# Kernel tuning notes

Measured on AMD Instinct MI355X. Metric: run time of the kernel, lower is better.

Reference implementation:

```python
import jax, jax.numpy as jnp
import numpy as np

B, N, F_IN, H = 1, 8192, 128, 64
NEG_INF = -1e9


def setup_inputs() -> dict:
    key = jax.random.key(0)
    ks = jax.random.split(key, 6)
    seq = jax.random.normal(ks[0], (B, N, F_IN), dtype=jnp.float32)
    # sparse-ish binary adjacency (~avg degree 64) with self loops
    adj = (jax.random.uniform(ks[1], (B, N, N)) < (64.0 / N)).astype(jnp.float32)
    eye = jnp.eye(N, dtype=jnp.float32)[None]
    adj = jnp.maximum(adj, eye)
    bias_mat = NEG_INF * (1.0 - adj)  # standard GAT bias mask
    W = jax.random.normal(ks[2], (F_IN, H), dtype=jnp.float32) * 0.08
    a1_w = jax.random.normal(ks[3], (H, 1), dtype=jnp.float32) * 0.1
    a2_w = jax.random.normal(ks[4], (H, 1), dtype=jnp.float32) * 0.1
    a1_b = jnp.zeros((1,), dtype=jnp.float32)
    a2_b = jnp.zeros((1,), dtype=jnp.float32)
    bias_zero = jnp.zeros((H,), dtype=jnp.float32)
    return {"seq": seq, "adj": adj, "bias_mat": bias_mat, "W": W,
            "a1_w": a1_w, "a1_b": a1_b, "a2_w": a2_w, "a2_b": a2_b,
            "bias_zero": bias_zero}


def reference(seq, adj, bias_mat, W, a1_w, a1_b, a2_w, a2_b, bias_zero):
    # Conv1D(kernel=1) == per-node linear projection
    seq_fts = jnp.einsum('bnf,fh->bnh', seq, W)          # [B,N,H]
    f1 = jnp.einsum('bnh,ho->bno', seq_fts, a1_w) + a1_b  # [B,N,1]
    f2 = jnp.einsum('bnh,ho->bno', seq_fts, a2_w) + a2_b  # [B,N,1]
    logits = f1 + jnp.swapaxes(f2, 1, 2)                  # [B,N,N] additive GAT logits
    # NOTE: module multiplies leaky_relu(logits) by dense adj, then adds bias_mat
    scores = jax.nn.leaky_relu(logits, 0.2) * adj + bias_mat
    coefs = jax.nn.softmax(scores, axis=-1)               # [B,N,N]
    vals = jnp.einsum('bnm,bmh->bnh', coefs, seq_fts)     # weighted aggregation
    ret = vals + bias_zero
    return jax.nn.elu(ret)
```

## Files before the change

### kernel.cpp

```cpp
#include <hip/hip_runtime.h>
#include <math.h>

#define NN 8192
#define FIN 128
#define HH 64
#define CAP 128
#define PROJ_BLOCKS 512
#define SCAN_BLOCKS 2048

typedef float f32x4 __attribute__((ext_vector_type(4)));
typedef const __attribute__((address_space(1))) unsigned int gu32;
typedef __attribute__((address_space(3))) unsigned int lu32;

__global__ __launch_bounds__(256) void proj_scan_kernel(
    const float* __restrict__ seq, const float* __restrict__ adj,
    const float* __restrict__ W,
    const float* __restrict__ a1_w, const float* __restrict__ a1_b,
    const float* __restrict__ a2_w, const float* __restrict__ a2_b,
    float* __restrict__ seq_fts, float* __restrict__ f1, float* __restrict__ f2,
    int* __restrict__ cnt_g, unsigned short* __restrict__ jb_g)
{
    __shared__ f32x4 stage[4][2][512];

    const int wave = threadIdx.x >> 6;
    const int lane = threadIdx.x & 63;
    const int b    = blockIdx.x;

    if ((b % 5) == 4) {
        const int base = (b / 5) * 16 + wave * 4;
        const float* __restrict__ s0 = seq + (size_t)(base + 0) * FIN;
        const float* __restrict__ s1 = seq + (size_t)(base + 1) * FIN;
        const float* __restrict__ s2 = seq + (size_t)(base + 2) * FIN;
        const float* __restrict__ s3 = seq + (size_t)(base + 3) * FIN;

        float a0 = 0.f, a1 = 0.f, a2 = 0.f, a3 = 0.f;
        #pragma unroll
        for (int f = 0; f < FIN; ++f) {
            const float wf = W[f * HH + lane];
            a0 = fmaf(s0[f], wf, a0);
            a1 = fmaf(s1[f], wf, a1);
            a2 = fmaf(s2[f], wf, a2);
            a3 = fmaf(s3[f], wf, a3);
        }
        seq_fts[(size_t)(base + 0) * HH + lane] = a0;
        seq_fts[(size_t)(base + 1) * HH + lane] = a1;
        seq_fts[(size_t)(base + 2) * HH + lane] = a2;
        seq_fts[(size_t)(base + 3) * HH + lane] = a3;

        const float w1 = a1_w[lane], w2 = a2_w[lane];
        float p10 = a0 * w1, p11 = a1 * w1, p12 = a2 * w1, p13 = a3 * w1;
        float p20 = a0 * w2, p21 = a1 * w2, p22 = a2 * w2, p23 = a3 * w2;
        #pragma unroll
        for (int off = 32; off >= 1; off >>= 1) {
            p10 += __shfl_xor(p10, off, 64);  p11 += __shfl_xor(p11, off, 64);
            p12 += __shfl_xor(p12, off, 64);  p13 += __shfl_xor(p13, off, 64);
            p20 += __shfl_xor(p20, off, 64);  p21 += __shfl_xor(p21, off, 64);
            p22 += __shfl_xor(p22, off, 64);  p23 += __shfl_xor(p23, off, 64);
        }
        if (lane == 0) {
            const float b1 = a1_b[0], b2 = a2_b[0];
            f1[base + 0] = p10 + b1;  f1[base + 1] = p11 + b1;
            f1[base + 2] = p12 + b1;  f1[base + 3] = p13 + b1;
            f2[base + 0] = p20 + b2;  f2[base + 1] = p21 + b2;
            f2[base + 2] = p22 + b2;  f2[base + 3] = p23 + b2;
        }
        return;
    }

    const int row = (b - b / 5) * 4 + wave;
    const char* __restrict__ g = (const char*)(adj + (size_t)row * NN);

    #define ISSUE(C_) do {                                                       \
        const char* src_ = g + (C_) * 8192 + lane * 16;                          \
        f32x4* dst_ = &stage[wave][(C_) & 1][0];                                 \
        _Pragma("unroll")                                                        \
        for (int i_ = 0; i_ < 8; ++i_) {                                         \
            __builtin_amdgcn_global_load_lds((gu32*)(src_ + i_ * 1024),          \
                                             (lu32*)((char*)dst_ + i_ * 1024),   \
                                             16, 0, 0);                          \
        }                                                                        \
    } while (0)

    #define PROCESS(C_, MW_) do {                                                \
        unsigned mw_ = 0;                                                        \
        _Pragma("unroll")                                                        \
        for (int i_ = 0; i_ < 8; ++i_) {                                         \
            const f32x4 a_ = stage[wave][(C_) & 1][i_ * 64 + lane];              \
            const unsigned bits_ = (unsigned)a_.x | ((unsigned)a_.y << 1)        \
                                 | ((unsigned)a_.z << 2) | ((unsigned)a_.w << 3);\
            mw_ |= bits_ << (i_ * 4);                                            \
        }                                                                        \
        (MW_) = mw_;                                                             \
    } while (0)

    #define WAITV(N_) do {                                                       \
        asm volatile("s_waitcnt vmcnt(" #N_ ")" ::: "memory");                   \
        __builtin_amdgcn_sched_barrier(0);                                       \
    } while (0)

    unsigned mask0, mask1, mask2, mask3;
    ISSUE(0); ISSUE(1);
    WAITV(8);
    PROCESS(0, mask0);
    __builtin_amdgcn_sched_barrier(0);
    ISSUE(2);
    WAITV(8);
    PROCESS(1, mask1);
    __builtin_amdgcn_sched_barrier(0);
    ISSUE(3);
    WAITV(8);
    PROCESS(2, mask2);
    WAITV(0);
    PROCESS(3, mask3);

    const int cnt = __popc(mask0) + __popc(mask1) + __popc(mask2) + __popc(mask3);
    int incl = cnt;
    #pragma unroll
    for (int off = 1; off < 64; off <<= 1) {
        const int u = __shfl_up(incl, off, 64);
        if (lane >= off) incl += u;
    }
    if (lane == 63) cnt_g[row] = incl;
    int p = incl - cnt;

    unsigned short* __restrict__ jrow = jb_g + (size_t)row * CAP;
    #define DECODE(MW, W_) do {                                              \
        unsigned m_ = (MW);                                                  \
        while (m_) {                                                         \
            const int b_ = __builtin_ctz(m_);  m_ &= m_ - 1;                 \
            const int j_ = ((((W_) * 8 + (b_ >> 2)) * 64 + lane) << 2) + (b_ & 3); \
            if (p < CAP) jrow[p] = (unsigned short)j_;                       \
            ++p;                                                             \
        }                                                                    \
    } while (0)
    DECODE(mask0, 0); DECODE(mask1, 1); DECODE(mask2, 2); DECODE(mask3, 3);
    #undef DECODE
    #undef ISSUE
    #undef PROCESS
    #undef WAITV
}

__global__ __launch_bounds__(256, 6) void gather_kernel(
    const float* __restrict__ seq_fts, const float* __restrict__ f1,
    const float* __restrict__ f2, const int* __restrict__ cnt_g,
    const unsigned short* __restrict__ jb_g,
    const float* __restrict__ bias_zero, float* __restrict__ out)
{
    const int wave = threadIdx.x >> 6;
    const int lane = threadIdx.x & 63;
    const int row  = blockIdx.x * 4 + wave;

    __shared__ int   jbuf[4][CAP];
    __shared__ float sbuf[4][CAP];

    const int n = min(cnt_g[row], CAP);
    const float f1i = f1[row];
    const unsigned short* __restrict__ jrow = jb_g + (size_t)row * CAP;

    float m = -1e30f;
    for (int q = lane; q < n; q += 64) {
        const int j = jrow[q];
        jbuf[wave][q] = j;
        const float x = f1i + f2[j];
        const float s = (x >= 0.f) ? x : 0.2f * x;
        sbuf[wave][q] = s;
        m = fmaxf(m, s);
    }
    #pragma unroll
    for (int off = 32; off >= 1; off >>= 1) m = fmaxf(m, __shfl_xor(m, off, 64));

    float d = 0.f;
    for (int q = lane; q < n; q += 64) {
        const float e = __expf(sbuf[wave][q] - m);
        sbuf[wave][q] = e;
        d += e;
    }
    #pragma unroll
    for (int off = 32; off >= 1; off >>= 1) d += __shfl_xor(d, off, 64);

    float acc0 = 0.f, acc1 = 0.f, acc2 = 0.f, acc3 = 0.f;
    float acc4 = 0.f, acc5 = 0.f, acc6 = 0.f, acc7 = 0.f;
    int q = 0;
    for (; q + 7 < n; q += 8) {
        acc0 = fmaf(sbuf[wave][q+0], seq_fts[(size_t)jbuf[wave][q+0] * HH + lane], acc0);
        acc1 = fmaf(sbuf[wave][q+1], seq_fts[(size_t)jbuf[wave][q+1] * HH + lane], acc1);
        acc2 = fmaf(sbuf[wave][q+2], seq_fts[(size_t)jbuf[wave][q+2] * HH + lane], acc2);
        acc3 = fmaf(sbuf[wave][q+3], seq_fts[(size_t)jbuf[wave][q+3] * HH + lane], acc3);
        acc4 = fmaf(sbuf[wave][q+4], seq_fts[(size_t)jbuf[wave][q+4] * HH + lane], acc4);
        acc5 = fmaf(sbuf[wave][q+5], seq_fts[(size_t)jbuf[wave][q+5] * HH + lane], acc5);
        acc6 = fmaf(sbuf[wave][q+6], seq_fts[(size_t)jbuf[wave][q+6] * HH + lane], acc6);
        acc7 = fmaf(sbuf[wave][q+7], seq_fts[(size_t)jbuf[wave][q+7] * HH + lane], acc7);
    }
    for (; q < n; ++q)
        acc0 = fmaf(sbuf[wave][q], seq_fts[(size_t)jbuf[wave][q] * HH + lane], acc0);

    const float v = (((acc0 + acc1) + (acc2 + acc3)) + ((acc4 + acc5) + (acc6 + acc7))) / d
                    + bias_zero[lane];
    out[(size_t)row * HH + lane] = (v > 0.f) ? v : expm1f(v);
}

extern "C" void kernel_launch(void* const* d_in, const int* in_sizes, int n_in,
                              void* d_out, int out_size, void* d_ws, size_t ws_size,
                              hipStream_t stream) {
    const float* seq       = (const float*)d_in[0];
    const float* adj       = (const float*)d_in[1];
    const float* W         = (const float*)d_in[3];
    const float* a1_w      = (const float*)d_in[4];
    const float* a1_b      = (const float*)d_in[5];
    const float* a2_w      = (const float*)d_in[6];
    const float* a2_b      = (const float*)d_in[7];
    const float* bias_zero = (const float*)d_in[8];
    float* out = (float*)d_out;

    char* ws = (char*)d_ws;
    float* seq_fts        = (float*)ws;
    float* f1             = (float*)(ws + 2097152);
    float* f2             = (float*)(ws + 2097152 + 32768);
    int*   cnt_g          = (int*)  (ws + 2097152 + 65536);
    unsigned short* jb_g  = (unsigned short*)(ws + 2097152 + 98304);

    proj_scan_kernel<<<PROJ_BLOCKS + SCAN_BLOCKS, 256, 0, stream>>>(
        seq, adj, W, a1_w, a1_b, a2_w, a2_b, seq_fts, f1, f2, cnt_g, jb_g);
    gather_kernel<<<NN / 4, 256, 0, stream>>>(
        seq_fts, f1, f2, cnt_g, jb_g, bias_zero, out);
}
```

Before: 61.44 us.

## Halve adjacency scan chunk size and deepen pipeline to eight stages

The adjacency row scan now stages 4 KB chunks per wave instead of 8 KB, halving the LDS footprint. It runs an eight-stage double-buffered pipeline and sets a nontemporal cache-policy bit on the global-to-LDS loads. Launch bounds now request 4 blocks per CU, aiming at higher occupancy and more loads in flight across waves for this bandwidth-bound scan. In exchange each wave has less per-wave load depth and more wait/process steps, and the bitmask decode index formula is rewritten to match the new chunk layout.

Result: slower. 69.89 us (+13.8%).

```diff
diff --git a/kernel.cpp b/kernel.cpp
--- a/kernel.cpp
+++ b/kernel.cpp
@@ -12,7 +12,7 @@
 typedef const __attribute__((address_space(1))) unsigned int gu32;
 typedef __attribute__((address_space(3))) unsigned int lu32;
 
-__global__ __launch_bounds__(256) void proj_scan_kernel(
+__global__ __launch_bounds__(256, 4) void proj_scan_kernel(
     const float* __restrict__ seq, const float* __restrict__ adj,
     const float* __restrict__ W,
     const float* __restrict__ a1_w, const float* __restrict__ a1_b,
@@ -20,7 +20,7 @@
     float* __restrict__ seq_fts, float* __restrict__ f1, float* __restrict__ f2,
     int* __restrict__ cnt_g, unsigned short* __restrict__ jb_g)
 {
-    __shared__ f32x4 stage[4][2][512];
+    __shared__ f32x4 stage[4][2][256];
 
     const int wave = threadIdx.x >> 6;
     const int lane = threadIdx.x & 63;
@@ -71,47 +71,49 @@
     const char* __restrict__ g = (const char*)(adj + (size_t)row * NN);
 
     #define ISSUE(C_) do {                                                       \
-        const char* src_ = g + (C_) * 8192 + lane * 16;                          \
-        f32x4* dst_ = &stage[wave][(C_) & 1][0];                                 \
+        const char* src_ = g + (C_) * 4096 + lane * 16;                          \
+        char* dst_ = (char*)&stage[wave][(C_) & 1][0];                           \
         _Pragma("unroll")                                                        \
-        for (int i_ = 0; i_ < 8; ++i_) {                                         \
+        for (int i_ = 0; i_ < 4; ++i_) {                                         \
             __builtin_amdgcn_global_load_lds((gu32*)(src_ + i_ * 1024),          \
-                                             (lu32*)((char*)dst_ + i_ * 1024),   \
-                                             16, 0, 0);                          \
+                                             (lu32*)(dst_ + i_ * 1024),          \
+                                             16, 0, 2 );                   \
         }                                                                        \
     } while (0)
 
-    #define PROCESS(C_, MW_) do {                                                \
-        unsigned mw_ = 0;                                                        \
+    #define PROCESS(C_, HW_) do {                                                \
+        unsigned hw_ = 0;                                                        \
         _Pragma("unroll")                                                        \
-        for (int i_ = 0; i_ < 8; ++i_) {                                         \
+        for (int i_ = 0; i_ < 4; ++i_) {                                         \
             const f32x4 a_ = stage[wave][(C_) & 1][i_ * 64 + lane];              \
             const unsigned bits_ = (unsigned)a_.x | ((unsigned)a_.y << 1)        \
                                  | ((unsigned)a_.z << 2) | ((unsigned)a_.w << 3);\
-            mw_ |= bits_ << (i_ * 4);                                            \
+            hw_ |= bits_ << (i_ * 4);                                            \
         }                                                                        \
-        (MW_) = mw_;                                                             \
+        (HW_) = hw_;                                                             \
     } while (0)
 
     #define WAITV(N_) do {                                                       \
         asm volatile("s_waitcnt vmcnt(" #N_ ")" ::: "memory");                   \
         __builtin_amdgcn_sched_barrier(0);                                       \
     } while (0)
-
-    unsigned mask0, mask1, mask2, mask3;
+    #define SB __builtin_amdgcn_sched_barrier(0)
+
+    unsigned h0, h1, h2, h3, h4, h5, h6, h7;
     ISSUE(0); ISSUE(1);
-    WAITV(8);
-    PROCESS(0, mask0);
-    __builtin_amdgcn_sched_barrier(0);
-    ISSUE(2);
-    WAITV(8);
-    PROCESS(1, mask1);
-    __builtin_amdgcn_sched_barrier(0);
-    ISSUE(3);
-    WAITV(8);
-    PROCESS(2, mask2);
-    WAITV(0);
-    PROCESS(3, mask3);
+    WAITV(4); PROCESS(0, h0); SB; ISSUE(2);
+    WAITV(4); PROCESS(1, h1); SB; ISSUE(3);
+    WAITV(4); PROCESS(2, h2); SB; ISSUE(4);
+    WAITV(4); PROCESS(3, h3); SB; ISSUE(5);
+    WAITV(4); PROCESS(4, h4); SB; ISSUE(6);
+    WAITV(4); PROCESS(5, h5); SB; ISSUE(7);
+    WAITV(4); PROCESS(6, h6);
+    WAITV(0); PROCESS(7, h7);
+
+    const unsigned mask0 = h0 | (h1 << 16);
+    const unsigned mask1 = h2 | (h3 << 16);
+    const unsigned mask2 = h4 | (h5 << 16);
+    const unsigned mask3 = h6 | (h7 << 16);
 
     const int cnt = __popc(mask0) + __popc(mask1) + __popc(mask2) + __popc(mask3);
     int incl = cnt;
@@ -124,20 +126,22 @@
     int p = incl - cnt;
 
     unsigned short* __restrict__ jrow = jb_g + (size_t)row * CAP;
-    #define DECODE(MW, W_) do {                                              \
-        unsigned m_ = (MW);                                                  \
-        while (m_) {                                                         \
-            const int b_ = __builtin_ctz(m_);  m_ &= m_ - 1;                 \
-            const int j_ = ((((W_) * 8 + (b_ >> 2)) * 64 + lane) << 2) + (b_ & 3); \
-            if (p < CAP) jrow[p] = (unsigned short)j_;                       \
-            ++p;                                                             \
-        }                                                                    \
+    #define DECODE(MW, W_) do {                                                  \
+        unsigned m_ = (MW);                                                      \
+        while (m_) {                                                             \
+            const int b_ = __builtin_ctz(m_);  m_ &= m_ - 1;                     \
+            const int j_ = ((((W_) * 512) + ((b_ >> 4) * 256)                    \
+                             + (((b_ >> 2) & 3) * 64) + lane) << 2) + (b_ & 3);  \
+            if (p < CAP) jrow[p] = (unsigned short)j_;                           \
+            ++p;                                                                 \
+        }                                                                        \
     } while (0)
     DECODE(mask0, 0); DECODE(mask1, 1); DECODE(mask2, 2); DECODE(mask3, 3);
     #undef DECODE
     #undef ISSUE
     #undef PROCESS
     #undef WAITV
+    #undef SB
 }
 
 __global__ __launch_bounds__(256, 6) void gather_kernel(
```

## Process two adjacency rows per wave with continuous prefetch pipeline and row swizzle

Applied to the files above, without the earlier changes.

Halves the fused kernel's grid by giving each scan wave two consecutive adjacency rows and each projection wave eight nodes. The double-buffered chunk pipeline runs across both rows, so the second row's loads are already in flight during the first row's prefix scan and index decode. Rows are also swizzled so consecutive blocks hit different 1024-row regions. The aim is to cut per-block launch overhead and pipeline bubbles on the dominant 256MB adjacency read, at the cost of fewer waves available to hide latency and more registers in the projection path.

Result: slower. 64.58 us (+5.1%).

```diff
diff --git a/kernel.cpp b/kernel.cpp
--- a/kernel.cpp
+++ b/kernel.cpp
@@ -5,8 +5,6 @@
 #define FIN 128
 #define HH 64
 #define CAP 128
-#define PROJ_BLOCKS 512
-#define SCAN_BLOCKS 2048
 
 typedef float f32x4 __attribute__((ext_vector_type(4)));
 typedef const __attribute__((address_space(1))) unsigned int gu32;
@@ -27,56 +25,47 @@
     const int b    = blockIdx.x;
 
     if ((b % 5) == 4) {
-        const int base = (b / 5) * 16 + wave * 4;
-        const float* __restrict__ s0 = seq + (size_t)(base + 0) * FIN;
-        const float* __restrict__ s1 = seq + (size_t)(base + 1) * FIN;
-        const float* __restrict__ s2 = seq + (size_t)(base + 2) * FIN;
-        const float* __restrict__ s3 = seq + (size_t)(base + 3) * FIN;
-
-        float a0 = 0.f, a1 = 0.f, a2 = 0.f, a3 = 0.f;
+        const int base = (b / 5) * 32 + wave * 8;
+        float acc[8];
+        #pragma unroll
+        for (int r = 0; r < 8; ++r) acc[r] = 0.f;
         #pragma unroll
         for (int f = 0; f < FIN; ++f) {
             const float wf = W[f * HH + lane];
-            a0 = fmaf(s0[f], wf, a0);
-            a1 = fmaf(s1[f], wf, a1);
-            a2 = fmaf(s2[f], wf, a2);
-            a3 = fmaf(s3[f], wf, a3);
+            #pragma unroll
+            for (int r = 0; r < 8; ++r)
+                acc[r] = fmaf(seq[(size_t)(base + r) * FIN + f], wf, acc[r]);
         }
-        seq_fts[(size_t)(base + 0) * HH + lane] = a0;
-        seq_fts[(size_t)(base + 1) * HH + lane] = a1;
-        seq_fts[(size_t)(base + 2) * HH + lane] = a2;
-        seq_fts[(size_t)(base + 3) * HH + lane] = a3;
+        #pragma unroll
+        for (int r = 0; r < 8; ++r)
+            seq_fts[(size_t)(base + r) * HH + lane] = acc[r];
 
         const float w1 = a1_w[lane], w2 = a2_w[lane];
-        float p10 = a0 * w1, p11 = a1 * w1, p12 = a2 * w1, p13 = a3 * w1;
-        float p20 = a0 * w2, p21 = a1 * w2, p22 = a2 * w2, p23 = a3 * w2;
-        #pragma unroll
-        for (int off = 32; off >= 1; off >>= 1) {
-            p10 += __shfl_xor(p10, off, 64);  p11 += __shfl_xor(p11, off, 64);
-            p12 += __shfl_xor(p12, off, 64);  p13 += __shfl_xor(p13, off, 64);
-            p20 += __shfl_xor(p20, off, 64);  p21 += __shfl_xor(p21, off, 64);
-            p22 += __shfl_xor(p22, off, 64);  p23 += __shfl_xor(p23, off, 64);
-        }
-        if (lane == 0) {
-            const float b1 = a1_b[0], b2 = a2_b[0];
-            f1[base + 0] = p10 + b1;  f1[base + 1] = p11 + b1;
-            f1[base + 2] = p12 + b1;  f1[base + 3] = p13 + b1;
-            f2[base + 0] = p20 + b2;  f2[base + 1] = p21 + b2;
-            f2[base + 2] = p22 + b2;  f2[base + 3] = p23 + b2;
+        const float b1 = a1_b[0],   b2 = a2_b[0];
+        #pragma unroll
+        for (int r = 0; r < 8; ++r) {
+            float v1 = acc[r] * w1, v2 = acc[r] * w2;
+            #pragma unroll
+            for (int off = 32; off >= 1; off >>= 1) {
+                v1 += __shfl_xor(v1, off, 64);
+                v2 += __shfl_xor(v2, off, 64);
+            }
+            if (lane == 0) { f1[base + r] = v1 + b1; f2[base + r] = v2 + b2; }
         }
         return;
     }
 
-    const int row = (b - b / 5) * 4 + wave;
-    const char* __restrict__ g = (const char*)(adj + (size_t)row * NN);
+    const int s    = b - b / 5;
+    const int row0 = (s & 7) * 1024 + (s >> 3) * 8 + wave * 2;
+    const char* __restrict__ g = (const char*)(adj + (size_t)row0 * NN);
 
     #define ISSUE(C_) do {                                                       \
         const char* src_ = g + (C_) * 8192 + lane * 16;                          \
-        f32x4* dst_ = &stage[wave][(C_) & 1][0];                                 \
+        char* dst_ = (char*)&stage[wave][(C_) & 1][0];                           \
         _Pragma("unroll")                                                        \
         for (int i_ = 0; i_ < 8; ++i_) {                                         \
             __builtin_amdgcn_global_load_lds((gu32*)(src_ + i_ * 1024),          \
-                                             (lu32*)((char*)dst_ + i_ * 1024),   \
+                                             (lu32*)(dst_ + i_ * 1024),          \
                                              16, 0, 0);                          \
         }                                                                        \
     } while (0)
@@ -97,47 +86,51 @@
         asm volatile("s_waitcnt vmcnt(" #N_ ")" ::: "memory");                   \
         __builtin_amdgcn_sched_barrier(0);                                       \
     } while (0)
-
-    unsigned mask0, mask1, mask2, mask3;
+    #define SB __builtin_amdgcn_sched_barrier(0)
+
+    auto finalize = [&](int row, unsigned mask0, unsigned mask1,
+                        unsigned mask2, unsigned mask3) {
+        const int cnt = __popc(mask0) + __popc(mask1) + __popc(mask2) + __popc(mask3);
+        int incl = cnt;
+        #pragma unroll
+        for (int off = 1; off < 64; off <<= 1) {
+            const int u = __shfl_up(incl, off, 64);
+            if (lane >= off) incl += u;
+        }
+        if (lane == 63) cnt_g[row] = incl;
+        int p = incl - cnt;
+        unsigned short* __restrict__ jrow = jb_g + (size_t)row * CAP;
+        #define DECODE(MW, W_) do {                                              \
+            unsigned m_ = (MW);                                                  \
+            while (m_) {                                                         \
+                const int b_ = __builtin_ctz(m_);  m_ &= m_ - 1;                 \
+                const int j_ = ((((W_) * 8 + (b_ >> 2)) * 64 + lane) << 2) + (b_ & 3); \
+                if (p < CAP) jrow[p] = (unsigned short)j_;                       \
+                ++p;                                                             \
+            }                                                                    \
+        } while (0)
+        DECODE(mask0, 0); DECODE(mask1, 1); DECODE(mask2, 2); DECODE(mask3, 3);
+        #undef DECODE
+    };
+
+    unsigned m0, m1, m2, m3, m4, m5, m6, m7;
     ISSUE(0); ISSUE(1);
-    WAITV(8);
-    PROCESS(0, mask0);
-    __builtin_amdgcn_sched_barrier(0);
-    ISSUE(2);
-    WAITV(8);
-    PROCESS(1, mask1);
-    __builtin_amdgcn_sched_barrier(0);
-    ISSUE(3);
-    WAITV(8);
-    PROCESS(2, mask2);
-    WAITV(0);
-    PROCESS(3, mask3);
-
-    const int cnt = __popc(mask0) + __popc(mask1) + __popc(mask2) + __popc(mask3);
-    int incl = cnt;
-    #pragma unroll
-    for (int off = 1; off < 64; off <<= 1) {
-        const int u = __shfl_up(incl, off, 64);
-        if (lane >= off) incl += u;
-    }
-    if (lane == 63) cnt_g[row] = incl;
-    int p = incl - cnt;
-
-    unsigned short* __restrict__ jrow = jb_g + (size_t)row * CAP;
-    #define DECODE(MW, W_) do {                                              \
-        unsigned m_ = (MW);                                                  \
-        while (m_) {                                                         \
-            const int b_ = __builtin_ctz(m_);  m_ &= m_ - 1;                 \
-            const int j_ = ((((W_) * 8 + (b_ >> 2)) * 64 + lane) << 2) + (b_ & 3); \
-            if (p < CAP) jrow[p] = (unsigned short)j_;                       \
-            ++p;                                                             \
-        }                                                                    \
-    } while (0)
-    DECODE(mask0, 0); DECODE(mask1, 1); DECODE(mask2, 2); DECODE(mask3, 3);
-    #undef DECODE
+    WAITV(8); PROCESS(0, m0); SB; ISSUE(2);
+    WAITV(8); PROCESS(1, m1); SB; ISSUE(3);
+    WAITV(8); PROCESS(2, m2); SB; ISSUE(4);
+    WAITV(8); PROCESS(3, m3); SB;
+    finalize(row0, m0, m1, m2, m3);
+    ISSUE(5);
+    WAITV(8); PROCESS(4, m4); SB; ISSUE(6);
+    WAITV(8); PROCESS(5, m5); SB; ISSUE(7);
+    WAITV(8); PROCESS(6, m6);
+    WAITV(0); PROCESS(7, m7);
+    finalize(row0 + 1, m4, m5, m6, m7);
+
     #undef ISSUE
     #undef PROCESS
     #undef WAITV
+    #undef SB
 }
 
 __global__ __launch_bounds__(256, 6) void gather_kernel(
@@ -219,7 +212,7 @@
     int*   cnt_g          = (int*)  (ws + 2097152 + 65536);
     unsigned short* jb_g  = (unsigned short*)(ws + 2097152 + 98304);
 
-    proj_scan_kernel<<<PROJ_BLOCKS + SCAN_BLOCKS, 256, 0, stream>>>(
+    proj_scan_kernel<<<1280, 256, 0, stream>>>(
         seq, adj, W, a1_w, a1_b, a2_w, a2_b, seq_fts, f1, f2, cnt_g, jb_g);
     gather_kernel<<<NN / 4, 256, 0, stream>>>(
         seq_fts, f1, f2, cnt_g, jb_g, bias_zero, out);
```
